# Performance work log

Hardware: AMD Instinct MI355X
Metric: run time of the kernel (lower is better)

The kernel has to match this reference:

```python
import jax, jax.numpy as jnp
import numpy as np

HIDDEN = 512


def setup_inputs() -> dict:
    key = jax.random.key(0)
    k1, k2, k3, k4, k5 = jax.random.split(key, 5)
    scale = 1.0 / np.sqrt(HIDDEN)
    return {
        "decoder_hidden": jax.random.normal(k1, (64, HIDDEN), dtype=jnp.float32),
        "encoder_outputs": jax.random.normal(k2, (4096, 64, HIDDEN), dtype=jnp.float32),
        "W1": jax.random.uniform(k3, (HIDDEN, HIDDEN), jnp.float32, -scale, scale),
        "W2": jax.random.uniform(k4, (HIDDEN, HIDDEN), jnp.float32, -scale, scale),
        "v": jax.random.uniform(k5, (HIDDEN,), jnp.float32, -scale, scale),
    }


def reference(decoder_hidden, encoder_outputs, W1, W2, v):
    # decoder_hidden: (B, H); encoder_outputs: (S, B, H)
    enc = jnp.transpose(encoder_outputs, (1, 0, 2))          # (B, S, H)
    dec_proj = decoder_hidden @ W1.T                          # (B, H) — no need to repeat over S
    enc_proj = jnp.einsum('bsh,gh->bsg', enc, W2)             # (B, S, H)
    energy = jnp.tanh(dec_proj[:, None, :] + enc_proj) @ v    # (B, S)
    attn_weights = jax.nn.softmax(energy, axis=1)             # (B, S)
    context = jnp.einsum('bs,bsh->bh', attn_weights, enc)     # (B, H)
    return (context, attn_weights)
```

## Files before the change

### kernel.cpp

```cpp
#include <hip/hip_runtime.h>
#include <math.h>


#define BATCH 64
#define SEQ   4096
#define HID   512

typedef __attribute__((ext_vector_type(8))) short bf16x8;
typedef __attribute__((ext_vector_type(4))) float f32x4;

__device__ __forceinline__ float fast_tanh(float x) {
    return 1.0f - 2.0f / (__expf(2.0f * x) + 1.0f);
}

__device__ __forceinline__ unsigned cvt2(float lo, float hi) {
    unsigned r;
    asm("v_cvt_pk_bf16_f32 %0, %1, %2" : "=v"(r) : "v"(lo), "v"(hi));
    return r;
}

__global__ void k_cvtW2(const float* __restrict__ W2, ushort* __restrict__ W2t)
{
    const int n  = blockIdx.x * 256 + threadIdx.x;
    const int g  = n >> 6, kc = n & 63;
    const int kb = kc >> 2, rgl = kc & 3;
    const int gh = g >> 8, wv = (g >> 6) & 3, fn = (g >> 4) & 3, gl = g & 15;

    const float* src = W2 + (size_t)g * HID + kc * 8;
    const float4 x = *reinterpret_cast<const float4*>(src);
    const float4 y = *reinterpret_cast<const float4*>(src + 4);
    uint4 u;
    u.x = cvt2(x.x, x.y);  u.y = cvt2(x.z, x.w);
    u.z = cvt2(y.x, y.y);  u.w = cvt2(y.z, y.w);

    const size_t dst = (size_t)gh * 131072 + kb * 8192 + wv * 2048 + fn * 512
                     + (rgl * 16 + gl) * 8;
    *reinterpret_cast<uint4*>(W2t + dst) = u;
}

__global__ void k_decproj(const float* __restrict__ dh,
                          const float* __restrict__ W1,
                          float* __restrict__ dp)
{
    __shared__ float wrow[HID];
    const int g = blockIdx.x;
    const int t = threadIdx.x;
    for (int i = t; i < HID; i += 256) wrow[i] = W1[g * HID + i];
    __syncthreads();

    const int b = t >> 2, q = t & 3;
    const float* dhb = dh + b * HID + q * 128;
    const float* wr  = wrow + q * 128;
    float acc = 0.f;
    #pragma unroll 8
    for (int i = 0; i < 128; i += 4) {
        const float4 d4 = *reinterpret_cast<const float4*>(dhb + i);
        acc = fmaf(d4.x, wr[i + 0], acc);
        acc = fmaf(d4.y, wr[i + 1], acc);
        acc = fmaf(d4.z, wr[i + 2], acc);
        acc = fmaf(d4.w, wr[i + 3], acc);
    }
    acc += __shfl_xor(acc, 1);
    acc += __shfl_xor(acc, 2);
    if (q == 0) dp[b * HID + g] = acc;
}

#define LDA 40

__global__ __launch_bounds__(256, 4)
void k_energy(const float* __restrict__ enc, const ushort* __restrict__ W2t,
              const float* __restrict__ dp,  const float* __restrict__ v,
              float* __restrict__ eparts)
{
    __shared__ __align__(16) ushort As[2][64 * LDA];
    __shared__ float part[4][64];

    const int idx  = blockIdx.x;
    const int g16  = idx >> 4, rr = idx & 15;
    const int gh   = rr >> 3;
    const int pair = (g16 << 3) | (rr & 7);
    const int schunk = pair & 63;
    const int b      = pair >> 6;
    const int s0     = schunk * 64;

    const int t    = threadIdx.x;
    const int lane = t & 63;
    const int wv   = t >> 6;
    const int gl   = lane & 15, rg = lane >> 4;

    f32x4 acc[4][4];
    const f32x4 z = {0.f, 0.f, 0.f, 0.f};
    #pragma unroll
    for (int m = 0; m < 4; ++m)
        #pragma unroll
        for (int n = 0; n < 4; ++n) acc[m][n] = z;

    const int arow = t >> 2, akq = t & 3;
    const float* aptr = enc + ((size_t)(s0 + arow) * BATCH + b) * HID + akq * 8;
    ushort* Aw0 = &As[0][arow * LDA + akq * 8];
    ushort* Aw1 = &As[1][arow * LDA + akq * 8];

    const ushort* Ap0 = &As[0][gl * LDA + rg * 8];
    const ushort* Ap1 = &As[1][gl * LDA + rg * 8];

    const ushort* bptr = W2t + (size_t)gh * 131072 + wv * 2048 + lane * 8;

    float4 a0 = *reinterpret_cast<const float4*>(aptr);
    float4 a1 = *reinterpret_cast<const float4*>(aptr + 4);
    {
        uint4 aw;
        aw.x = cvt2(a0.x, a0.y);  aw.y = cvt2(a0.z, a0.w);
        aw.z = cvt2(a1.x, a1.y);  aw.w = cvt2(a1.z, a1.w);
        *reinterpret_cast<uint4*>(Aw0) = aw;
    }
    a0 = *reinterpret_cast<const float4*>(aptr + 32);
    a1 = *reinterpret_cast<const float4*>(aptr + 36);
    __syncthreads();

    #pragma unroll
    for (int kb = 0; kb < 16; ++kb) {
        bf16x8 bfr[4];
        #pragma unroll
        for (int n = 0; n < 4; ++n)
            bfr[n] = *reinterpret_cast<const bf16x8*>(bptr + kb * 8192 + n * 512);

        const ushort* Ap = (kb & 1) ? Ap1 : Ap0;
        bf16x8 af[4];
        #pragma unroll
        for (int m = 0; m < 4; ++m)
            af[m] = *reinterpret_cast<const bf16x8*>(Ap + m * 16 * LDA);

        if (kb < 15) {
            uint4 aw;
            aw.x = cvt2(a0.x, a0.y);  aw.y = cvt2(a0.z, a0.w);
            aw.z = cvt2(a1.x, a1.y);  aw.w = cvt2(a1.z, a1.w);
            *reinterpret_cast<uint4*>((kb & 1) ? Aw0 : Aw1) = aw;
        }
        if (kb < 14) {
            a0 = *reinterpret_cast<const float4*>(aptr + (kb + 2) * 32);
            a1 = *reinterpret_cast<const float4*>(aptr + (kb + 2) * 32 + 4);
        }

        #pragma unroll
        for (int m = 0; m < 4; ++m)
            #pragma unroll
            for (int n = 0; n < 4; ++n)
                acc[m][n] = __builtin_amdgcn_mfma_f32_16x16x32_bf16(
                    af[m], bfr[n], acc[m][n], 0, 0, 0);

        __syncthreads();
    }

    float dpv[4], vv[4];
    #pragma unroll
    for (int n = 0; n < 4; ++n) {
        const int g = gh * 256 + wv * 64 + n * 16 + gl;
        dpv[n] = dp[b * HID + g];
        vv[n]  = v[g];
    }
    float p[4][4];
    #pragma unroll
    for (int m = 0; m < 4; ++m)
        #pragma unroll
        for (int r = 0; r < 4; ++r) p[m][r] = 0.f;
    #pragma unroll
    for (int n = 0; n < 4; ++n)
        #pragma unroll
        for (int m = 0; m < 4; ++m)
            #pragma unroll
            for (int r = 0; r < 4; ++r)
                p[m][r] += fast_tanh(dpv[n] + acc[m][n][r]) * vv[n];

    #pragma unroll
    for (int m = 0; m < 4; ++m)
        #pragma unroll
        for (int r = 0; r < 4; ++r) {
            float x = p[m][r];
            x += __shfl_xor(x, 1);
            x += __shfl_xor(x, 2);
            x += __shfl_xor(x, 4);
            x += __shfl_xor(x, 8);
            p[m][r] = x;
        }
    if (gl == 0) {
        #pragma unroll
        for (int m = 0; m < 4; ++m)
            #pragma unroll
            for (int r = 0; r < 4; ++r)
                part[wv][m * 16 + rg * 4 + r] = p[m][r];
    }
    __syncthreads();

    if (t < 64) {
        const float e = part[0][t] + part[1][t] + part[2][t] + part[3][t];
        eparts[(size_t)gh * BATCH * SEQ + (size_t)b * SEQ + s0 + t] = e;
    }
}

__global__ void k_softmax(const float* __restrict__ eparts,
                          float* __restrict__ attn)
{
    __shared__ float redm[4], reds[4];
    const int b = blockIdx.x, t = threadIdx.x;
    const float* e0 = eparts + (size_t)b * SEQ;
    const float* e1 = eparts + (size_t)BATCH * SEQ + (size_t)b * SEQ;

    float4 ev[4];
    float m = -3.4e38f;
    #pragma unroll
    for (int i = 0; i < 4; ++i) {
        const float4 x = *reinterpret_cast<const float4*>(e0 + i * 1024 + t * 4);
        const float4 y = *reinterpret_cast<const float4*>(e1 + i * 1024 + t * 4);
        ev[i] = make_float4(x.x + y.x, x.y + y.y, x.z + y.z, x.w + y.w);
        m = fmaxf(m, fmaxf(fmaxf(ev[i].x, ev[i].y), fmaxf(ev[i].z, ev[i].w)));
    }
    #pragma unroll
    for (int off = 1; off < 64; off <<= 1) m = fmaxf(m, __shfl_xor(m, off));
    if ((t & 63) == 0) redm[t >> 6] = m;
    __syncthreads();
    m = fmaxf(fmaxf(redm[0], redm[1]), fmaxf(redm[2], redm[3]));

    float s = 0.f;
    #pragma unroll
    for (int i = 0; i < 4; ++i) {
        ev[i].x = __expf(ev[i].x - m);  ev[i].y = __expf(ev[i].y - m);
        ev[i].z = __expf(ev[i].z - m);  ev[i].w = __expf(ev[i].w - m);
        s += (ev[i].x + ev[i].y) + (ev[i].z + ev[i].w);
    }
    #pragma unroll
    for (int off = 1; off < 64; off <<= 1) s += __shfl_xor(s, off);
    if ((t & 63) == 0) reds[t >> 6] = s;
    __syncthreads();
    s = (reds[0] + reds[1]) + (reds[2] + reds[3]);
    const float inv = 1.0f / s;

    float* o = attn + (size_t)b * SEQ;
    #pragma unroll
    for (int i = 0; i < 4; ++i) {
        const float4 w4 = make_float4(ev[i].x * inv, ev[i].y * inv,
                                      ev[i].z * inv, ev[i].w * inv);
        *reinterpret_cast<float4*>(o + i * 1024 + t * 4) = w4;
    }
}

__global__ void k_ctxpart(const float* __restrict__ enc,
                          const float* __restrict__ attn,
                          float* __restrict__ pctx)
{
    __shared__ float w[256];
    const int b  = blockIdx.x;
    const int sp = blockIdx.y;
    const int t  = threadIdx.x;

    w[t] = attn[(size_t)b * SEQ + sp * 256 + t];
    __syncthreads();

    const float2* e2 = reinterpret_cast<const float2*>(enc);
    size_t idx = ((size_t)sp * 256 * BATCH + b) * (HID / 2) + t;
    const size_t stride = (size_t)BATCH * (HID / 2);

    float ax = 0.f, ay = 0.f;
    #pragma unroll 4
    for (int s = 0; s < 256; ++s) {
        const float2 ev = e2[idx];
        const float ws = w[s];
        ax = fmaf(ws, ev.x, ax);
        ay = fmaf(ws, ev.y, ay);
        idx += stride;
    }
    float2* p2 = reinterpret_cast<float2*>(pctx);
    p2[((size_t)sp * BATCH + b) * (HID / 2) + t] = make_float2(ax, ay);
}

__global__ void k_ctxsum(const float* __restrict__ pctx,
                         float* __restrict__ ctx)
{
    const int i = blockIdx.x * 256 + threadIdx.x;
    float s = 0.f;
    #pragma unroll
    for (int sp = 0; sp < 16; ++sp) s += pctx[(size_t)sp * BATCH * HID + i];
    ctx[i] = s;
}

extern "C" void kernel_launch(void* const* d_in, const int* in_sizes, int n_in,
                              void* d_out, int out_size, void* d_ws, size_t ws_size,
                              hipStream_t stream)
{
    const float* dh  = (const float*)d_in[0];
    const float* enc = (const float*)d_in[1];
    const float* W1  = (const float*)d_in[2];
    const float* W2  = (const float*)d_in[3];
    const float* v   = (const float*)d_in[4];

    float* out  = (float*)d_out;
    float* ctx  = out;
    float* attn = out + BATCH * HID;

    float*  dp      = (float*)d_ws;
    ushort* W2t     = (ushort*)(dp + BATCH * HID);
    float*  shared2 = (float*)(W2t + HID * HID);
    float*  eparts  = shared2;
    float*  pctx    = shared2;

    k_cvtW2  <<<128, 256, 0, stream>>>(W2, W2t);
    k_decproj<<<HID, 256, 0, stream>>>(dh, W1, dp);
    k_energy <<<8192, 256, 0, stream>>>(enc, W2t, dp, v, eparts);
    k_softmax<<<BATCH, 256, 0, stream>>>(eparts, attn);
    k_ctxpart<<<dim3(BATCH, 16), 256, 0, stream>>>(enc, attn, pctx);
    k_ctxsum <<<BATCH * HID / 256, 256, 0, stream>>>(pctx, ctx);
}
```

Baseline: 328.0 us.

## Load encoder A-fragments directly from global memory, dropping LDS staging and barriers

```diff
diff --git a/kernel.cpp b/kernel.cpp
--- a/kernel.cpp
+++ b/kernel.cpp
@@ -18,6 +18,8 @@
     asm("v_cvt_pk_bf16_f32 %0, %1, %2" : "=v"(r) : "v"(lo), "v"(hi));
     return r;
 }
+
+union bfpack { uint4 u; bf16x8 v; };
 
 __global__ void k_cvtW2(const float* __restrict__ W2, ushort* __restrict__ W2t)
 {
@@ -65,14 +67,11 @@
     if (q == 0) dp[b * HID + g] = acc;
 }
 
-#define LDA 40
-
 __global__ __launch_bounds__(256, 4)
 void k_energy(const float* __restrict__ enc, const ushort* __restrict__ W2t,
               const float* __restrict__ dp,  const float* __restrict__ v,
               float* __restrict__ eparts)
 {
-    __shared__ __align__(16) ushort As[2][64 * LDA];
     __shared__ float part[4][64];
 
     const int idx  = blockIdx.x;
@@ -95,27 +94,10 @@
         #pragma unroll
         for (int n = 0; n < 4; ++n) acc[m][n] = z;
 
-    const int arow = t >> 2, akq = t & 3;
-    const float* aptr = enc + ((size_t)(s0 + arow) * BATCH + b) * HID + akq * 8;
-    ushort* Aw0 = &As[0][arow * LDA + akq * 8];
-    ushort* Aw1 = &As[1][arow * LDA + akq * 8];
-
-    const ushort* Ap0 = &As[0][gl * LDA + rg * 8];
-    const ushort* Ap1 = &As[1][gl * LDA + rg * 8];
+    const float* a0 = enc + ((size_t)(s0 + gl) * BATCH + b) * HID + rg * 8;
+    #define ASTRIDE_M ((size_t)16 * BATCH * HID)
 
     const ushort* bptr = W2t + (size_t)gh * 131072 + wv * 2048 + lane * 8;
-
-    float4 a0 = *reinterpret_cast<const float4*>(aptr);
-    float4 a1 = *reinterpret_cast<const float4*>(aptr + 4);
-    {
-        uint4 aw;
-        aw.x = cvt2(a0.x, a0.y);  aw.y = cvt2(a0.z, a0.w);
-        aw.z = cvt2(a1.x, a1.y);  aw.w = cvt2(a1.z, a1.w);
-        *reinterpret_cast<uint4*>(Aw0) = aw;
-    }
-    a0 = *reinterpret_cast<const float4*>(aptr + 32);
-    a1 = *reinterpret_cast<const float4*>(aptr + 36);
-    __syncthreads();
 
     #pragma unroll
     for (int kb = 0; kb < 16; ++kb) {
@@ -124,21 +106,16 @@
         for (int n = 0; n < 4; ++n)
             bfr[n] = *reinterpret_cast<const bf16x8*>(bptr + kb * 8192 + n * 512);
 
-        const ushort* Ap = (kb & 1) ? Ap1 : Ap0;
         bf16x8 af[4];
         #pragma unroll
-        for (int m = 0; m < 4; ++m)
-            af[m] = *reinterpret_cast<const bf16x8*>(Ap + m * 16 * LDA);
-
-        if (kb < 15) {
-            uint4 aw;
-            aw.x = cvt2(a0.x, a0.y);  aw.y = cvt2(a0.z, a0.w);
-            aw.z = cvt2(a1.x, a1.y);  aw.w = cvt2(a1.z, a1.w);
-            *reinterpret_cast<uint4*>((kb & 1) ? Aw0 : Aw1) = aw;
-        }
-        if (kb < 14) {
-            a0 = *reinterpret_cast<const float4*>(aptr + (kb + 2) * 32);
-            a1 = *reinterpret_cast<const float4*>(aptr + (kb + 2) * 32 + 4);
+        for (int m = 0; m < 4; ++m) {
+            const float* ap = a0 + m * ASTRIDE_M + kb * 32;
+            const float4 x = *reinterpret_cast<const float4*>(ap);
+            const float4 y = *reinterpret_cast<const float4*>(ap + 4);
+            bfpack w;
+            w.u.x = cvt2(x.x, x.y);  w.u.y = cvt2(x.z, x.w);
+            w.u.z = cvt2(y.x, y.y);  w.u.w = cvt2(y.z, y.w);
+            af[m] = w.v;
         }
 
         #pragma unroll
@@ -147,8 +124,6 @@
             for (int n = 0; n < 4; ++n)
                 acc[m][n] = __builtin_amdgcn_mfma_f32_16x16x32_bf16(
                     af[m], bfr[n], acc[m][n], 0, 0, 0);
-
-        __syncthreads();
     }
 
     float dpv[4], vv[4];
```

After: 702.5 us. 2.14x slower.
